# Performance work log

Hardware: AMD Instinct MI355X
Metric: run time of the kernel (lower is better)

The kernel has to match this reference:

```python
import jax, jax.numpy as jnp
import numpy as np

T, B, D, BF = 512, 256, 256, 2  # time (nodes/tree), batch, feature dim, branching factor


def setup_inputs() -> dict:
    key = jax.random.key(0)
    k1, k2, k3 = jax.random.split(key, 3)
    inputs = jax.random.normal(k1, (T, B, D), dtype=jnp.float32)
    # Valid postfix (shift-reduce) arity sequence: two leaves, then alternate
    # combine(2)/leaf(0) -> left-comb binary tree; keeps stack pointer in range.
    t = np.arange(T)
    ar = np.where((t >= 2) & (t % 2 == 0), 2, 0).astype(np.int64)
    arities = jnp.asarray(np.broadcast_to(ar[:, None], (T, B)))
    scale = 1.0 / np.sqrt(D)
    W_in = jax.random.normal(k2, (D, D), dtype=jnp.float32) * scale
    W_ch = jax.random.normal(k3, (BF, D, D), dtype=jnp.float32) * scale
    b = jnp.zeros((D,), dtype=jnp.float32)
    return {"inputs": inputs, "arities": arities, "W_in": W_in, "W_ch": W_ch, "b": b}


def reference(inputs, arities, W_in, W_ch, b):
    Tn, Bn, Dn = inputs.shape
    bf = W_ch.shape[0]
    k = jnp.arange(Bn)

    def unit(x, children):
        # tree-RNN cell: tanh(x@W_in + sum_i child_i@W_ch[i] + b)
        h = x @ W_in + b
        for i in range(bf):
            h = h + children[i] @ W_ch[i]
        return jnp.tanh(h)

    memory0 = jnp.zeros((Tn, Bn, Dn), dtype=inputs.dtype)
    stack0 = jnp.zeros((Bn, Tn + bf), dtype=arities.dtype)
    ptr0 = jnp.full((Bn,), bf - 1, dtype=arities.dtype)

    def step(carry, xs):
        memory, stack, ptr = carry
        x_t, ar, t = xs
        children = []
        for i in range(bf):
            idx = stack[k, ptr - i]                    # [B] top-of-stack pointers
            entry = memory[idx, k]                     # [B, D] gather child features
            mask = (ar > i).astype(entry.dtype)[:, None]
            children.append(entry * mask)              # zero absent children
        new_entry = unit(x_t, children)
        memory = memory.at[t].set(new_entry)           # scatter to memory slot t
        ptr = ptr - jnp.abs(ar) + 1                    # pop arity, push 1
        ignore = ar == -1
        # stack[k,ptr] *= ignore; += t*(1-ignore)  <=>  keep old if ignore else t
        stack = stack.at[k, ptr].set(jnp.where(ignore, stack[k, ptr], t))
        return (memory, stack, ptr), None

    (memory, stack, ptr), _ = jax.lax.scan(
        step, (memory0, stack0, ptr0), (inputs, arities, jnp.arange(Tn)))
    out = memory[stack[k, ptr], k]                     # [B, D] tree roots
    return (out, memory)
```

## Files before the change

kernel.cpp:

```cpp
#include <hip/hip_runtime.h>
#include <hip/hip_bf16.h>


constexpr int T = 512, B = 256, D = 256;

constexpr int WS_CNT  = 0;
constexpr int WS_ROOT = 16;
constexpr int WS_NW   = 272;
constexpr int WS_L0   = 1024;
constexpr int WS_L1   = WS_L0 + T * B;
constexpr int WS_WORK = WS_L1 + T * B;

__global__ __launch_bounds__(256) void k_stack(const int* __restrict__ ar,
                                               unsigned* __restrict__ ws) {
  __shared__ int ar_l[T];
  __shared__ int S[1024];
  __shared__ unsigned lbuf0[T];
  __shared__ unsigned lbuf1[T];
  __shared__ unsigned wbuf[1024];
  __shared__ int cnts[4];
  __shared__ unsigned base0, base1;

  int k = blockIdx.x;
  int tid = threadIdx.x;
  ar_l[tid]       = ar[tid * B + k];
  ar_l[tid + 256] = ar[(tid + 256) * B + k];
  S[tid] = 0; S[tid + 256] = 0; S[tid + 512] = 0; S[tid + 768] = 0;
  __syncthreads();

  if (tid == 0) {
    int ptr = 1;
    int top = 0, next = 0;
    int n0 = 0, n1 = 0, nw = 0;
    for (int t = 0; t < T; t++) {
      int a = ar_l[t];
      int aa = a < 0 ? -a : a;
      unsigned cc[2]; int ncc = 0;
      if (a > 0) {
        int c0 = top;
        if (ar_l[c0] <= 0)
          lbuf0[n0++] = (unsigned)c0 | ((unsigned)t << 9) | ((unsigned)k << 18);
        else
          cc[ncc++] = (unsigned)c0;
        if (a > 1) {
          int c1 = next;
          if (ar_l[c1] <= 0)
            lbuf1[n1++] = (unsigned)c1 | ((unsigned)t << 9) | ((unsigned)k << 18);
          else
            cc[ncc++] = (unsigned)c1 | (1u << 18);
        }
      }
      if (a >= 1) {
        if (ncc == 0) {
          wbuf[nw++] = (unsigned)t | (1u << 19) | (1u << 20);
        } else {
          for (int e = 0; e < ncc; e++) {
            unsigned w = (unsigned)t | ((cc[e] & 511u) << 9) |
                         (((cc[e] >> 18) & 1u) << 18) | (1u << 21);
            if (e == 0) w |= (1u << 19);
            if (e == ncc - 1) w |= (1u << 20);
            wbuf[nw++] = w;
          }
        }
      }
      int pnew = ptr - aa + 1;
      if (a != -1) {
        S[pnew & 1023] = t;
        if (aa == 0)      { next = top; top = t; }
        else if (aa == 1) { top = t; }
        else              { top = t; next = S[(pnew - 1) & 1023]; }
      }
      ptr = pnew;
    }
    cnts[0] = n0; cnts[1] = n1; cnts[2] = nw;
    cnts[3] = S[ptr & 1023];
    base0 = atomicAdd(ws + WS_CNT + 0, (unsigned)n0);
    base1 = atomicAdd(ws + WS_CNT + 1, (unsigned)n1);
  }
  __syncthreads();
  int n0 = cnts[0], n1 = cnts[1], nw = cnts[2];
  for (int i = tid; i < n0; i += 256) ws[WS_L0 + base0 + i] = lbuf0[i];
  for (int i = tid; i < n1; i += 256) ws[WS_L1 + base1 + i] = lbuf1[i];
  for (int i = tid; i < nw; i += 256) ws[WS_WORK + k * 1024 + i] = wbuf[i];
  if (tid == 0) { ws[WS_NW + k] = (unsigned)nw; ws[WS_ROOT + k] = (unsigned)cnts[3]; }
}

__global__ __launch_bounds__(256) void k_gemm_h(const float* __restrict__ X,
                                                const float* __restrict__ W,
                                                const float* __restrict__ bias,
                                                float* __restrict__ Hm) {
  int row0 = blockIdx.x * 64;
  __shared__ float As[16][65];
  __shared__ float Bs[16][256];
  int tid = threadIdx.x;
  int cq = tid & 31, rg = tid >> 5;
  float acc[8][8];
#pragma unroll
  for (int q = 0; q < 8; q++) {
    float bv = bias[cq + 32 * q];
#pragma unroll
    for (int rr = 0; rr < 8; rr++) acc[rr][q] = bv;
  }
  int sr = tid >> 2;
  int skc = (tid & 3) * 4;
  for (int kk = 0; kk < 256; kk += 16) {
    float4 a4 = *(const float4*)&X[(row0 + sr) * 256 + kk + skc];
    As[skc + 0][sr] = a4.x; As[skc + 1][sr] = a4.y;
    As[skc + 2][sr] = a4.z; As[skc + 3][sr] = a4.w;
#pragma unroll
    for (int r = 0; r < 16; r++) Bs[r][tid] = W[(kk + r) * 256 + tid];
    __syncthreads();
#pragma unroll
    for (int kc = 0; kc < 16; kc++) {
      float a[8], bb[8];
#pragma unroll
      for (int rr = 0; rr < 8; rr++) a[rr] = As[kc][rg * 8 + rr];
#pragma unroll
      for (int q = 0; q < 8; q++) bb[q] = Bs[kc][cq + 32 * q];
#pragma unroll
      for (int rr = 0; rr < 8; rr++)
#pragma unroll
        for (int q = 0; q < 8; q++) acc[rr][q] += a[rr] * bb[q];
    }
    __syncthreads();
  }
#pragma unroll
  for (int rr = 0; rr < 8; rr++)
#pragma unroll
    for (int q = 0; q < 8; q++)
      Hm[(row0 + rg * 8 + rr) * 256 + cq + 32 * q] = acc[rr][q];
}

__global__ __launch_bounds__(256) void k_leafgemm(const float* __restrict__ Hm,
                                                  float* __restrict__ Gm,
                                                  const float* __restrict__ Wch,
                                                  const unsigned* __restrict__ list,
                                                  const unsigned* __restrict__ cntp,
                                                  int which) {
  unsigned cnt = *cntp;
  unsigned tile0 = blockIdx.x * 64;
  if (tile0 >= cnt) return;
  int ne = (int)min(64u, cnt - tile0);
  __shared__ unsigned ent[64];
  __shared__ float As[16][65];
  __shared__ float Bs[16][256];
  int tid = threadIdx.x;
  if (tid < 64) ent[tid] = (tid < ne) ? list[tile0 + tid] : 0u;
  __syncthreads();
  const float* W = Wch + which * (D * D);
  int cq = tid & 31, rg = tid >> 5;
  float acc[8][8];
#pragma unroll
  for (int rr = 0; rr < 8; rr++)
#pragma unroll
    for (int q = 0; q < 8; q++) acc[rr][q] = 0.0f;
  int sr = tid >> 2;
  int skc = (tid & 3) * 4;
  unsigned se = ent[sr];
  int sc = (int)(se & 511u), skb = (int)((se >> 18) & 255u);
  const float* srow = &Hm[((sc << 8) + skb) * 256];
  for (int kk = 0; kk < 256; kk += 16) {
    float4 a4;
    if (sr < ne) a4 = *(const float4*)&srow[kk + skc];
    else { a4.x = a4.y = a4.z = a4.w = 0.0f; }
    As[skc + 0][sr] = tanhf(a4.x); As[skc + 1][sr] = tanhf(a4.y);
    As[skc + 2][sr] = tanhf(a4.z); As[skc + 3][sr] = tanhf(a4.w);
#pragma unroll
    for (int r = 0; r < 16; r++) Bs[r][tid] = W[(kk + r) * 256 + tid];
    __syncthreads();
#pragma unroll
    for (int kc = 0; kc < 16; kc++) {
      float a[8], bb[8];
#pragma unroll
      for (int rr = 0; rr < 8; rr++) a[rr] = As[kc][rg * 8 + rr];
#pragma unroll
      for (int q = 0; q < 8; q++) bb[q] = Bs[kc][cq + 32 * q];
#pragma unroll
      for (int rr = 0; rr < 8; rr++)
#pragma unroll
        for (int q = 0; q < 8; q++) acc[rr][q] += a[rr] * bb[q];
    }
    __syncthreads();
  }
#pragma unroll
  for (int rr = 0; rr < 8; rr++) {
    int e = rg * 8 + rr;
    if (e < ne) {
      unsigned en = ent[e];
      int t = (int)((en >> 9) & 511u), kb = (int)((en >> 18) & 255u);
      float* dst = &Gm[((t << 8) + kb) * 256];
#pragma unroll
      for (int q = 0; q < 8; q++) dst[cq + 32 * q] += acc[rr][q];
    }
  }
}

__global__ __launch_bounds__(256) void k_leaftanh(const int* __restrict__ ar,
                                                  float* __restrict__ Mm) {
  int r0 = blockIdx.x * 64;
  __shared__ int lar[64];
  int tid = threadIdx.x;
  if (tid < 64) lar[tid] = ar[r0 + tid];
  __syncthreads();
  for (int r = 0; r < 64; r++) {
    if (lar[r] <= 0) {
      float v = Mm[(r0 + r) * 256 + tid];
      Mm[(r0 + r) * 256 + tid] = tanhf(v);
    }
  }
}

__global__ __launch_bounds__(512) void k_seq(float* __restrict__ Mm,
                                             const float* __restrict__ Wch,
                                             const unsigned* __restrict__ ws) {
  int k = blockIdx.x;
  int tid = threadIdx.x;
  int j = tid & 255, h = tid >> 8;
  __shared__ __align__(16) float crow[256];
  __shared__ float partial[256];
  __shared__ int cached;
  if (tid == 0) cached = -1;
  float w[128];
  const float* W1 = Wch + D * D;
#pragma unroll
  for (int p = 0; p < 128; p++) w[p] = W1[(h * 128 + p) * 256 + j];
  int nw = (int)ws[WS_NW + k];
  const unsigned* work = ws + WS_WORK + k * 1024;
  float acc = 0.0f;
  __syncthreads();
  for (int n = 0; n < nw; n++) {
    unsigned e = work[n];
    int t = (int)(e & 511u), c = (int)((e >> 9) & 511u);
    int wi = (int)((e >> 18) & 1u);
    bool first = (e >> 19) & 1u, last = (e >> 20) & 1u, hasc = (e >> 21) & 1u;
    if (first) acc = (h == 0) ? Mm[((t << 8) + k) * 256 + j] : 0.0f;
    if (hasc) {
      if (c != cached) {
        __syncthreads();
        if (tid < 256) crow[tid] = Mm[((c << 8) + k) * 256 + tid];
        if (tid == 0) cached = c;
        __syncthreads();
      }
      if (wi == 1) {
#pragma unroll
        for (int p = 0; p < 32; p++) {
          float4 c4 = ((const float4*)crow)[h * 32 + p];
          acc += c4.x * w[4 * p] + c4.y * w[4 * p + 1] +
                 c4.z * w[4 * p + 2] + c4.w * w[4 * p + 3];
        }
      } else {
        const float* W0 = Wch;
#pragma unroll 8
        for (int p = 0; p < 128; p++)
          acc += crow[h * 128 + p] * W0[(h * 128 + p) * 256 + j];
      }
    }
    if (last) {
      if (h == 1) partial[j] = acc;
      __syncthreads();
      if (h == 0) {
        float v = tanhf(acc + partial[j]);
        Mm[((t << 8) + k) * 256 + j] = v;
        crow[j] = v;
      }
      if (tid == 0) cached = t;
      __syncthreads();
    }
  }
}

__global__ __launch_bounds__(256) void k_root(const float* __restrict__ Mm,
                                              float* __restrict__ out,
                                              const unsigned* __restrict__ ws) {
  int k = blockIdx.x;
  unsigned r = ws[WS_ROOT + k];
  out[k * 256 + threadIdx.x] = Mm[(((int)r << 8) + k) * 256 + threadIdx.x];
}

extern "C" void kernel_launch(void* const* d_in, const int* in_sizes, int n_in,
                              void* d_out, int out_size, void* d_ws, size_t ws_size,
                              hipStream_t stream) {
  const float* X    = (const float*)d_in[0];
  const int*   AR   = (const int*)d_in[1];
  const float* Win  = (const float*)d_in[2];
  const float* Wch  = (const float*)d_in[3];
  const float* bias = (const float*)d_in[4];
  float* out = (float*)d_out;
  float* Mm  = out + B * D;
  unsigned* ws = (unsigned*)d_ws;

  hipMemsetAsync(d_ws, 0, 512, stream);
  k_stack<<<B, 256, 0, stream>>>(AR, ws);
  k_gemm_h<<<(T * B) / 64, 256, 0, stream>>>(X, Win, bias, Mm);
  k_leafgemm<<<(T * B) / 64, 256, 0, stream>>>(Mm, Mm, Wch, ws + WS_L0, ws + WS_CNT + 0, 0);
  k_leafgemm<<<(T * B) / 64, 256, 0, stream>>>(Mm, Mm, Wch, ws + WS_L1, ws + WS_CNT + 1, 1);
  k_leaftanh<<<(T * B) / 64, 256, 0, stream>>>(AR, Mm);
  k_seq<<<B, 512, 0, stream>>>(Mm, Wch, ws);
  k_root<<<B, 256, 0, stream>>>(Mm, out, ws);
}
```

Measured before the change: 1.075 ms.

## Register-prefetch GEMM tiles, vectorize LDS access, and prefetch work entries in sequential kernel

After: 1.545 ms. 43.7% more time.

```diff
diff --git a/kernel.cpp b/kernel.cpp
--- a/kernel.cpp
+++ b/kernel.cpp
@@ -85,65 +85,97 @@
   if (tid == 0) { ws[WS_NW + k] = (unsigned)nw; ws[WS_ROOT + k] = (unsigned)cnts[3]; }
 }
 
-__global__ __launch_bounds__(256) void k_gemm_h(const float* __restrict__ X,
-                                                const float* __restrict__ W,
-                                                const float* __restrict__ bias,
-                                                float* __restrict__ Hm) {
+__global__ __launch_bounds__(256, 3) void k_gemm_h(const float* __restrict__ X,
+                                                   const float* __restrict__ W,
+                                                   const float* __restrict__ bias,
+                                                   float* __restrict__ Hm) {
   int row0 = blockIdx.x * 64;
-  __shared__ float As[16][65];
-  __shared__ float Bs[16][256];
+  __shared__ __align__(16) float As[16][72];
+  __shared__ __align__(16) float Bs[16][256];
   int tid = threadIdx.x;
   int cq = tid & 31, rg = tid >> 5;
   float acc[8][8];
-#pragma unroll
-  for (int q = 0; q < 8; q++) {
-    float bv = bias[cq + 32 * q];
-#pragma unroll
-    for (int rr = 0; rr < 8; rr++) acc[rr][q] = bv;
+  float4 b_lo = *(const float4*)&bias[cq * 4];
+  float4 b_hi = *(const float4*)&bias[128 + cq * 4];
+#pragma unroll
+  for (int rr = 0; rr < 8; rr++) {
+    acc[rr][0] = b_lo.x; acc[rr][1] = b_lo.y; acc[rr][2] = b_lo.z; acc[rr][3] = b_lo.w;
+    acc[rr][4] = b_hi.x; acc[rr][5] = b_hi.y; acc[rr][6] = b_hi.z; acc[rr][7] = b_hi.w;
   }
   int sr = tid >> 2;
   int skc = (tid & 3) * 4;
+  float4 pa;
+  float4 pb[4];
+  pa = *(const float4*)&X[(row0 + sr) * 256 + skc];
+#pragma unroll
+  for (int i = 0; i < 4; i++) {
+    int idx = tid + i * 256;
+    int r = idx >> 6, c4 = idx & 63;
+    pb[i] = *(const float4*)&W[r * 256 + c4 * 4];
+  }
   for (int kk = 0; kk < 256; kk += 16) {
-    float4 a4 = *(const float4*)&X[(row0 + sr) * 256 + kk + skc];
-    As[skc + 0][sr] = a4.x; As[skc + 1][sr] = a4.y;
-    As[skc + 2][sr] = a4.z; As[skc + 3][sr] = a4.w;
-#pragma unroll
-    for (int r = 0; r < 16; r++) Bs[r][tid] = W[(kk + r) * 256 + tid];
-    __syncthreads();
+    As[skc + 0][sr] = pa.x; As[skc + 1][sr] = pa.y;
+    As[skc + 2][sr] = pa.z; As[skc + 3][sr] = pa.w;
+#pragma unroll
+    for (int i = 0; i < 4; i++) {
+      int idx = tid + i * 256;
+      int r = idx >> 6, c4 = idx & 63;
+      *(float4*)&Bs[r][c4 * 4] = pb[i];
+    }
+    __builtin_amdgcn_sched_barrier(0);
+    asm volatile("s_waitcnt lgkmcnt(0)" ::: "memory");
+    __builtin_amdgcn_s_barrier();
+    __builtin_amdgcn_sched_barrier(0);
+    if (kk + 16 < 256) {
+      pa = *(const float4*)&X[(row0 + sr) * 256 + kk + 16 + skc];
+#pragma unroll
+      for (int i = 0; i < 4; i++) {
+        int idx = tid + i * 256;
+        int r = idx >> 6, c4 = idx & 63;
+        pb[i] = *(const float4*)&W[(kk + 16 + r) * 256 + c4 * 4];
+      }
+    }
 #pragma unroll
     for (int kc = 0; kc < 16; kc++) {
-      float a[8], bb[8];
-#pragma unroll
-      for (int rr = 0; rr < 8; rr++) a[rr] = As[kc][rg * 8 + rr];
-#pragma unroll
-      for (int q = 0; q < 8; q++) bb[q] = Bs[kc][cq + 32 * q];
+      float4 a0  = *(const float4*)&As[kc][rg * 8];
+      float4 a1  = *(const float4*)&As[kc][rg * 8 + 4];
+      float4 blo = *(const float4*)&Bs[kc][cq * 4];
+      float4 bhi = *(const float4*)&Bs[kc][128 + cq * 4];
+      float a[8]  = {a0.x, a0.y, a0.z, a0.w, a1.x, a1.y, a1.z, a1.w};
+      float bb[8] = {blo.x, blo.y, blo.z, blo.w, bhi.x, bhi.y, bhi.z, bhi.w};
 #pragma unroll
       for (int rr = 0; rr < 8; rr++)
 #pragma unroll
         for (int q = 0; q < 8; q++) acc[rr][q] += a[rr] * bb[q];
     }
-    __syncthreads();
-  }
-#pragma unroll
-  for (int rr = 0; rr < 8; rr++)
-#pragma unroll
-    for (int q = 0; q < 8; q++)
-      Hm[(row0 + rg * 8 + rr) * 256 + cq + 32 * q] = acc[rr][q];
-}
-
-__global__ __launch_bounds__(256) void k_leafgemm(const float* __restrict__ Hm,
-                                                  float* __restrict__ Gm,
-                                                  const float* __restrict__ Wch,
-                                                  const unsigned* __restrict__ list,
-                                                  const unsigned* __restrict__ cntp,
-                                                  int which) {
+    __builtin_amdgcn_sched_barrier(0);
+    __builtin_amdgcn_s_barrier();
+    __builtin_amdgcn_sched_barrier(0);
+  }
+#pragma unroll
+  for (int rr = 0; rr < 8; rr++) {
+    float4 lo, hi;
+    lo.x = acc[rr][0]; lo.y = acc[rr][1]; lo.z = acc[rr][2]; lo.w = acc[rr][3];
+    hi.x = acc[rr][4]; hi.y = acc[rr][5]; hi.z = acc[rr][6]; hi.w = acc[rr][7];
+    float* dst = &Hm[(row0 + rg * 8 + rr) * 256];
+    *(float4*)&dst[cq * 4] = lo;
+    *(float4*)&dst[128 + cq * 4] = hi;
+  }
+}
+
+__global__ __launch_bounds__(256, 3) void k_leafgemm(const float* __restrict__ Hm,
+                                                     float* __restrict__ Gm,
+                                                     const float* __restrict__ Wch,
+                                                     const unsigned* __restrict__ list,
+                                                     const unsigned* __restrict__ cntp,
+                                                     int which) {
   unsigned cnt = *cntp;
   unsigned tile0 = blockIdx.x * 64;
   if (tile0 >= cnt) return;
   int ne = (int)min(64u, cnt - tile0);
   __shared__ unsigned ent[64];
-  __shared__ float As[16][65];
-  __shared__ float Bs[16][256];
+  __shared__ __align__(16) float As[16][72];
+  __shared__ __align__(16) float Bs[16][256];
   int tid = threadIdx.x;
   if (tid < 64) ent[tid] = (tid < ne) ? list[tile0 + tid] : 0u;
   __syncthreads();
@@ -159,28 +191,53 @@
   unsigned se = ent[sr];
   int sc = (int)(se & 511u), skb = (int)((se >> 18) & 255u);
   const float* srow = &Hm[((sc << 8) + skb) * 256];
+  float4 pa; pa.x = pa.y = pa.z = pa.w = 0.0f;
+  float4 pb[4];
+  if (sr < ne) pa = *(const float4*)&srow[skc];
+#pragma unroll
+  for (int i = 0; i < 4; i++) {
+    int idx = tid + i * 256;
+    int r = idx >> 6, c4 = idx & 63;
+    pb[i] = *(const float4*)&W[r * 256 + c4 * 4];
+  }
   for (int kk = 0; kk < 256; kk += 16) {
-    float4 a4;
-    if (sr < ne) a4 = *(const float4*)&srow[kk + skc];
-    else { a4.x = a4.y = a4.z = a4.w = 0.0f; }
-    As[skc + 0][sr] = tanhf(a4.x); As[skc + 1][sr] = tanhf(a4.y);
-    As[skc + 2][sr] = tanhf(a4.z); As[skc + 3][sr] = tanhf(a4.w);
-#pragma unroll
-    for (int r = 0; r < 16; r++) Bs[r][tid] = W[(kk + r) * 256 + tid];
-    __syncthreads();
+    As[skc + 0][sr] = tanhf(pa.x); As[skc + 1][sr] = tanhf(pa.y);
+    As[skc + 2][sr] = tanhf(pa.z); As[skc + 3][sr] = tanhf(pa.w);
+#pragma unroll
+    for (int i = 0; i < 4; i++) {
+      int idx = tid + i * 256;
+      int r = idx >> 6, c4 = idx & 63;
+      *(float4*)&Bs[r][c4 * 4] = pb[i];
+    }
+    __builtin_amdgcn_sched_barrier(0);
+    asm volatile("s_waitcnt lgkmcnt(0)" ::: "memory");
+    __builtin_amdgcn_s_barrier();
+    __builtin_amdgcn_sched_barrier(0);
+    if (kk + 16 < 256) {
+      if (sr < ne) pa = *(const float4*)&srow[kk + 16 + skc];
+#pragma unroll
+      for (int i = 0; i < 4; i++) {
+        int idx = tid + i * 256;
+        int r = idx >> 6, c4 = idx & 63;
+        pb[i] = *(const float4*)&W[(kk + 16 + r) * 256 + c4 * 4];
+      }
+    }
 #pragma unroll
     for (int kc = 0; kc < 16; kc++) {
-      float a[8], bb[8];
-#pragma unroll
-      for (int rr = 0; rr < 8; rr++) a[rr] = As[kc][rg * 8 + rr];
-#pragma unroll
-      for (int q = 0; q < 8; q++) bb[q] = Bs[kc][cq + 32 * q];
+      float4 a0  = *(const float4*)&As[kc][rg * 8];
+      float4 a1  = *(const float4*)&As[kc][rg * 8 + 4];
+      float4 blo = *(const float4*)&Bs[kc][cq * 4];
+      float4 bhi = *(const float4*)&Bs[kc][128 + cq * 4];
+      float a[8]  = {a0.x, a0.y, a0.z, a0.w, a1.x, a1.y, a1.z, a1.w};
+      float bb[8] = {blo.x, blo.y, blo.z, blo.w, bhi.x, bhi.y, bhi.z, bhi.w};
 #pragma unroll
       for (int rr = 0; rr < 8; rr++)
 #pragma unroll
         for (int q = 0; q < 8; q++) acc[rr][q] += a[rr] * bb[q];
     }
-    __syncthreads();
+    __builtin_amdgcn_sched_barrier(0);
+    __builtin_amdgcn_s_barrier();
+    __builtin_amdgcn_sched_barrier(0);
   }
 #pragma unroll
   for (int rr = 0; rr < 8; rr++) {
@@ -189,8 +246,12 @@
       unsigned en = ent[e];
       int t = (int)((en >> 9) & 511u), kb = (int)((en >> 18) & 255u);
       float* dst = &Gm[((t << 8) + kb) * 256];
-#pragma unroll
-      for (int q = 0; q < 8; q++) dst[cq + 32 * q] += acc[rr][q];
+      float4 lo = *(const float4*)&dst[cq * 4];
+      float4 hi = *(const float4*)&dst[128 + cq * 4];
+      lo.x += acc[rr][0]; lo.y += acc[rr][1]; lo.z += acc[rr][2]; lo.w += acc[rr][3];
+      hi.x += acc[rr][4]; hi.y += acc[rr][5]; hi.z += acc[rr][6]; hi.w += acc[rr][7];
+      *(float4*)&dst[cq * 4] = lo;
+      *(float4*)&dst[128 + cq * 4] = hi;
     }
   }
 }
@@ -210,9 +271,9 @@
   }
 }
 
-__global__ __launch_bounds__(512) void k_seq(float* __restrict__ Mm,
-                                             const float* __restrict__ Wch,
-                                             const unsigned* __restrict__ ws) {
+__global__ __launch_bounds__(512, 2) void k_seq(float* __restrict__ Mm,
+                                                const float* __restrict__ Wch,
+                                                const unsigned* __restrict__ ws) {
   int k = blockIdx.x;
   int tid = threadIdx.x;
   int j = tid & 255, h = tid >> 8;
@@ -228,18 +289,30 @@
   const unsigned* work = ws + WS_WORK + k * 1024;
   float acc = 0.0f;
   __syncthreads();
+  unsigned e = (nw > 0) ? work[0] : 0u;
+  float nb = 0.0f;
+  if (nw > 0 && ((e >> 19) & 1u) && h == 0)
+    nb = Mm[(((int)(e & 511u) << 8) + k) * 256 + j];
   for (int n = 0; n < nw; n++) {
-    unsigned e = work[n];
-    int t = (int)(e & 511u), c = (int)((e >> 9) & 511u);
-    int wi = (int)((e >> 18) & 1u);
-    bool first = (e >> 19) & 1u, last = (e >> 20) & 1u, hasc = (e >> 21) & 1u;
-    if (first) acc = (h == 0) ? Mm[((t << 8) + k) * 256 + j] : 0.0f;
+    unsigned cur = e;
+    unsigned nxt = (n + 1 < nw) ? work[n + 1] : 0u;
+    int t = (int)(cur & 511u), c = (int)((cur >> 9) & 511u);
+    int wi = (int)((cur >> 18) & 1u);
+    bool first = (cur >> 19) & 1u, last = (cur >> 20) & 1u, hasc = (cur >> 21) & 1u;
+    if (first) acc = (h == 0) ? nb : 0.0f;
+    float nb2 = 0.0f;
+    if ((n + 1 < nw) && ((nxt >> 19) & 1u) && h == 0)
+      nb2 = Mm[(((int)(nxt & 511u) << 8) + k) * 256 + j];
     if (hasc) {
       if (c != cached) {
-        __syncthreads();
+        asm volatile("s_waitcnt vmcnt(0) lgkmcnt(0)" ::: "memory");
+        __builtin_amdgcn_s_barrier();
+        __builtin_amdgcn_sched_barrier(0);
         if (tid < 256) crow[tid] = Mm[((c << 8) + k) * 256 + tid];
         if (tid == 0) cached = c;
-        __syncthreads();
+        asm volatile("s_waitcnt vmcnt(0) lgkmcnt(0)" ::: "memory");
+        __builtin_amdgcn_s_barrier();
+        __builtin_amdgcn_sched_barrier(0);
       }
       if (wi == 1) {
 #pragma unroll
@@ -257,15 +330,22 @@
     }
     if (last) {
       if (h == 1) partial[j] = acc;
-      __syncthreads();
+      __builtin_amdgcn_sched_barrier(0);
+      asm volatile("s_waitcnt lgkmcnt(0)" ::: "memory");
+      __builtin_amdgcn_s_barrier();
+      __builtin_amdgcn_sched_barrier(0);
       if (h == 0) {
         float v = tanhf(acc + partial[j]);
         Mm[((t << 8) + k) * 256 + j] = v;
         crow[j] = v;
       }
       if (tid == 0) cached = t;
-      __syncthreads();
-    }
+      __builtin_amdgcn_sched_barrier(0);
+      asm volatile("s_waitcnt lgkmcnt(0)" ::: "memory");
+      __builtin_amdgcn_s_barrier();
+      __builtin_amdgcn_sched_barrier(0);
+    }
+    e = nxt; nb = nb2;
   }
 }
 
```
